# Performance work log

Hardware: AMD Instinct MI355X
Metric: run time of the kernel (lower is better)

Reference implementation:

```python
import jax, jax.numpy as jnp
import numpy as np

B, L, WD = 4096, 30, 300          # batch of news, title length, word dim
H, AD = 20, 20                    # attention heads, per-head dim
MD = H * AD                       # multi_dim = 400
E, ED = 10, 100                   # entities per news, entity dim
QD = 200                          # query_vector_dim
CAT, CD = 18, 50                  # category vocab / dim
SUB, SD = 300, 50                 # subcategory vocab / dim


def _mha(x, wq, bq, wk, bk, wv, bv):
    # x: [B, L, Din] -> [B, L, MD]; standard multi-head self-attention
    b, l, _ = x.shape
    q = (x @ wq + bq).reshape(b, l, H, AD)
    k = (x @ wk + bk).reshape(b, l, H, AD)
    v = (x @ wv + bv).reshape(b, l, H, AD)
    scores = jnp.einsum('blhd,bmhd->bhlm', q, k) / jnp.sqrt(jnp.asarray(AD, x.dtype))
    attn = jax.nn.softmax(scores, axis=-1)
    out = jnp.einsum('bhlm,bmhd->blhd', attn, v)
    return out.reshape(b, l, MD)


def _layernorm(x, g, b):
    mu = jnp.mean(x, axis=-1, keepdims=True)
    var = jnp.var(x, axis=-1, keepdims=True)
    return (x - mu) / jnp.sqrt(var + 1e-5) * g + b


def _additive(x, w, b, q):
    # x: [B, L, D] -> [B, D]
    scores = jnp.tanh(x @ w + b) @ q            # [B, L]
    alpha = jax.nn.softmax(scores, axis=-1)
    return jnp.einsum('bl,bld->bd', alpha, x)


def setup_inputs() -> dict:
    key = jax.random.key(0)
    ks = iter(jax.random.split(key, 40))
    n = lambda shape, s=0.02: (jax.random.normal(next(ks), shape, dtype=jnp.float32) * s)
    inp = {
        'word_embedding': jax.random.normal(next(ks), (B, L, WD), dtype=jnp.float32),
        'entity_embedding': jax.random.normal(next(ks), (B, E, ED), dtype=jnp.float32),
        'category_index': jax.random.randint(next(ks), (B,), 0, CAT, dtype=jnp.int64 if jax.config.jax_enable_x64 else jnp.int32),
        'subcategory_index': jax.random.randint(next(ks), (B,), 0, SUB, dtype=jnp.int64 if jax.config.jax_enable_x64 else jnp.int32),
        # category / subcategory branches
        'emb_cat': n((CAT, CD), 1.0), 'fc1_w': n((CD, MD)), 'fc1_b': jnp.zeros((MD,), jnp.float32),
        'emb_sub': n((SUB, SD), 1.0), 'fc2_w': n((SD, MD)), 'fc2_b': jnp.zeros((MD,), jnp.float32),
        # word multi-head self-attention
        'wq': n((WD, MD)), 'bq': jnp.zeros((MD,), jnp.float32),
        'wk': n((WD, MD)), 'bk': jnp.zeros((MD,), jnp.float32),
        'wv': n((WD, MD)), 'bv': jnp.zeros((MD,), jnp.float32),
        # shared LayerNorm
        'ln_g': jnp.ones((MD,), jnp.float32), 'ln_b': jnp.zeros((MD,), jnp.float32),
        # word additive attention
        'wa_w': n((MD, QD)), 'wa_b': jnp.zeros((QD,), jnp.float32), 'wa_q': n((QD,), 1.0),
        # entity branch: fc3 + GCN (learnable adjacency over the E entities of a news)
        'fc3_w': n((ED, ED)), 'fc3_b': jnp.zeros((ED,), jnp.float32),
        'gcn_A': n((E, E), 1.0), 'gcn_w': n((ED, MD)), 'gcn_b': jnp.zeros((MD,), jnp.float32),
        'ea_w': n((MD, QD)), 'ea_b': jnp.zeros((QD,), jnp.float32), 'ea_q': n((QD,), 1.0),
        # final news-level additive attention over 4 views
        'na_w': n((MD, QD)), 'na_b': jnp.zeros((QD,), jnp.float32), 'na_q': n((QD,), 1.0),
    }
    return inp


def reference(word_embedding, entity_embedding, category_index, subcategory_index,
              emb_cat, fc1_w, fc1_b, emb_sub, fc2_w, fc2_b,
              wq, bq, wk, bk, wv, bv, ln_g, ln_b,
              wa_w, wa_b, wa_q, fc3_w, fc3_b, gcn_A, gcn_w, gcn_b,
              ea_w, ea_b, ea_q, na_w, na_b, na_q):
    # category / subcategory reps (dropout is identity in eval)
    cat_rep = jnp.tanh(emb_cat[category_index] @ fc1_w + fc1_b)      # [B, MD]
    sub_rep = jnp.tanh(emb_sub[subcategory_index] @ fc2_w + fc2_b)   # [B, MD]
    # word branch
    w = _mha(word_embedding, wq, bq, wk, bk, wv, bv)                 # [B, L, MD]
    w = _layernorm(w, ln_g, ln_b)
    word_rep = jnp.tanh(_additive(w, wa_w, wa_b, wa_q))              # [B, MD]
    # entity branch: fc3 -> intra-news GCN -> shared LayerNorm
    e = jnp.tanh(entity_embedding @ fc3_w + fc3_b)                   # [B, E, ED]
    e = jax.nn.relu(jnp.einsum('ef,bfd->bed', gcn_A, e) @ gcn_w + gcn_b)  # [B, E, MD]
    e = _layernorm(e, ln_g, ln_b)
    ent_rep = jnp.tanh(_additive(e, ea_w, ea_b, ea_q))               # [B, MD]
    # fuse the 4 views with additive attention
    views = jnp.stack([word_rep, ent_rep, cat_rep, sub_rep], axis=1)  # [B, 4, MD]
    news_rep = jnp.tanh(_additive(views, na_w, na_b, na_q))          # [B, MD]
    return news_rep
```

## Files before the change

### kernel.cpp

```cpp
#include <hip/hip_runtime.h>
#include <hip/hip_bf16.h>
#include <math.h>

#define B_  4096
#define L_  30
#define WD_ 300
#define H_  20
#define AD_ 20
#define MD_ 400
#define E_  10
#define ED_ 100
#define QD_ 200
#define CD_ 50
#define SD_ 50

typedef unsigned short ushort_t;
typedef __attribute__((ext_vector_type(8))) short bf16x8_t;
typedef __attribute__((ext_vector_type(4))) float f32x4_t;

#define SX_STR   328
#define QKV_STR  1218
#define OUTB_STR 424
#define SOUT_STR 401
#define P_STR    33
#define WT_K     320
#define WAT_K    416

#define N_WT    (1200 * WT_K)
#define N_WAT   (208 * WAT_K)
#define N_FC3T  (112 * 128)
#define N_GCNT  (400 * 128)
#define N_EAT   (208 * WAT_K)

union FragU {
  unsigned  u[4];
  short     s[8];
  bf16x8_t  h;
};

__device__ __forceinline__ ushort_t f2bf(float f) {
  unsigned u = __builtin_bit_cast(unsigned, f);
  unsigned r = (u + 0x7fffu + ((u >> 16) & 1u)) >> 16;
  return (ushort_t)r;
}
__device__ __forceinline__ float bf2f(ushort_t h) {
  return __builtin_bit_cast(float, ((unsigned)h) << 16);
}
__device__ __forceinline__ float wave_reduce_sum(float v) {
  #pragma unroll
  for (int off = 32; off > 0; off >>= 1) v += __shfl_xor(v, off);
  return v;
}
__device__ __forceinline__ void split2(float v, ushort_t* __restrict__ H,
                                       ushort_t* __restrict__ Lo, int idx) {
  const ushort_t h = f2bf(v);
  H[idx] = h;
  Lo[idx] = f2bf(v - bf2f(h));
}

__global__ __launch_bounds__(256) void prep_weights(
    const float* __restrict__ wq, const float* __restrict__ wk, const float* __restrict__ wv,
    const float* __restrict__ wa_w, const float* __restrict__ fc3_w,
    const float* __restrict__ gcn_w, const float* __restrict__ ea_w,
    ushort_t* __restrict__ Wt,
    ushort_t* __restrict__ WatH, ushort_t* __restrict__ WatL,
    ushort_t* __restrict__ fc3TH, ushort_t* __restrict__ fc3TL,
    ushort_t* __restrict__ gcnTH, ushort_t* __restrict__ gcnTL,
    ushort_t* __restrict__ eaTH, ushort_t* __restrict__ eaTL)
{
  int idx = blockIdx.x * 256 + threadIdx.x;
  if (idx < N_WT) {
    const int n = idx / WT_K, k = idx - n * WT_K;
    float v = 0.f;
    if (k < WD_) {
      const float* w = (n < 400) ? wq : (n < 800) ? wk : wv;
      const int c = (n < 400) ? n : (n < 800) ? n - 400 : n - 800;
      v = w[k * MD_ + c];
    }
    Wt[idx] = f2bf(v);
    return;
  }
  idx -= N_WT;
  if (idx < N_WAT) {
    const int q = idx / WAT_K, d = idx - q * WAT_K;
    const float v = (q < QD_ && d < MD_) ? wa_w[d * QD_ + q] : 0.f;
    split2(v, WatH, WatL, idx);
    return;
  }
  idx -= N_WAT;
  if (idx < N_FC3T) {
    const int n = idx / 128, k = idx - n * 128;
    const float v = (n < ED_ && k < ED_) ? fc3_w[k * ED_ + n] : 0.f;
    split2(v, fc3TH, fc3TL, idx);
    return;
  }
  idx -= N_FC3T;
  if (idx < N_GCNT) {
    const int n = idx / 128, k = idx - n * 128;
    const float v = (k < ED_) ? gcn_w[k * MD_ + n] : 0.f;
    split2(v, gcnTH, gcnTL, idx);
    return;
  }
  idx -= N_GCNT;
  if (idx < N_EAT) {
    const int q = idx / WAT_K, d = idx - q * WAT_K;
    const float v = (q < QD_ && d < MD_) ? ea_w[d * QD_ + q] : 0.f;
    split2(v, eaTH, eaTL, idx);
  }
}

__global__ __launch_bounds__(512) void word_branch_kernel(
    const float* __restrict__ X,
    const ushort_t* __restrict__ Wt,
    const ushort_t* __restrict__ WatH, const ushort_t* __restrict__ WatL,
    const float* __restrict__ bq, const float* __restrict__ bk, const float* __restrict__ bv,
    const float* __restrict__ ln_g, const float* __restrict__ ln_b,
    const float* __restrict__ wa_b, const float* __restrict__ wa_q,
    float* __restrict__ word_rep)
{
  __shared__ __align__(16) union {
    ushort_t x[32 * SX_STR];
    float    p[8 * 32 * P_STR];
  } uA;
  __shared__ __align__(16) union {
    ushort_t qkv[32 * QKV_STR];
    struct { ushort_t h[32 * OUTB_STR], l[32 * OUTB_STR]; } o;
  } uB;
  __shared__ __align__(16) float sOut[30 * SOUT_STR];
  __shared__ float sSc[32];
  __shared__ float sAlpha[32];

  const int b    = blockIdx.x;
  const int tid  = threadIdx.x;
  const int wave = tid >> 6;
  const int lane = tid & 63;
  const int lr   = lane & 15;
  const int kg   = lane >> 4;

  const float* xb = X + (size_t)b * (L_ * WD_);
  {
    const int r = tid >> 4, c0 = tid & 15;
    #pragma unroll
    for (int k = 0; k < 20; ++k) {
      const int c = c0 + k * 16;
      const float v = (r < L_ && c < WD_) ? xb[r * WD_ + c] : 0.f;
      uA.x[r * SX_STR + c] = f2bf(v);
    }
  }
  if (tid < 32) sSc[tid] = 0.f;
  __syncthreads();

  for (int jt = wave; jt < 38; jt += 8) {
    const int nt0 = 2 * jt, nt1 = 2 * jt + 1;
    const bool has1 = (nt1 < 75);
    f32x4_t a00 = {0,0,0,0}, a10 = {0,0,0,0}, a01 = {0,0,0,0}, a11 = {0,0,0,0};
    for (int ks = 0; ks < 10; ++ks) {
      const int kb = ks * 32 + kg * 8;
      bf16x8_t af0 = *reinterpret_cast<const bf16x8_t*>(&uA.x[lr * SX_STR + kb]);
      bf16x8_t af1 = *reinterpret_cast<const bf16x8_t*>(&uA.x[(16 + lr) * SX_STR + kb]);
      bf16x8_t bf0 = *reinterpret_cast<const bf16x8_t*>(&Wt[(nt0 * 16 + lr) * WT_K + kb]);
      a00 = __builtin_amdgcn_mfma_f32_16x16x32_bf16(af0, bf0, a00, 0, 0, 0);
      a10 = __builtin_amdgcn_mfma_f32_16x16x32_bf16(af1, bf0, a10, 0, 0, 0);
      if (has1) {
        bf16x8_t bf1 = *reinterpret_cast<const bf16x8_t*>(&Wt[(nt1 * 16 + lr) * WT_K + kb]);
        a01 = __builtin_amdgcn_mfma_f32_16x16x32_bf16(af0, bf1, a01, 0, 0, 0);
        a11 = __builtin_amdgcn_mfma_f32_16x16x32_bf16(af1, bf1, a11, 0, 0, 0);
      }
    }
    #pragma unroll
    for (int half = 0; half < 2; ++half) {
      if (half && !has1) break;
      const int nt = half ? nt1 : nt0;
      const int col = nt * 16 + lr;
      const float bias = (col < 400) ? bq[col] : (col < 800) ? bk[col - 400] : bv[col - 800];
      const f32x4_t am0 = half ? a01 : a00;
      const f32x4_t am1 = half ? a11 : a10;
      #pragma unroll
      for (int i = 0; i < 4; ++i) {
        uB.qkv[(kg * 4 + i) * QKV_STR + col]      = f2bf(am0[i] + bias);
        uB.qkv[(16 + kg * 4 + i) * QKV_STR + col] = f2bf(am1[i] + bias);
      }
    }
  }
  __syncthreads();

  float* pw = &uA.p[wave * (32 * P_STR)];
  for (int h = wave; h < H_; h += 8) {
    const int hq = h * AD_, hk = 400 + h * AD_, hv = 800 + h * AD_;

    bf16x8_t aq[2], bkf[2];
    #pragma unroll
    for (int t = 0; t < 2; ++t) {
      FragU fq, fk;
      fq.u[0]=fq.u[1]=fq.u[2]=fq.u[3]=0;
      fk.u[0]=fk.u[1]=fk.u[2]=fk.u[3]=0;
      if (kg < 3) {
        const ushort_t* pq = &uB.qkv[(t * 16 + lr) * QKV_STR + hq + kg * 8];
        const ushort_t* pk = &uB.qkv[(t * 16 + lr) * QKV_STR + hk + kg * 8];
        fq.u[0] = *(const unsigned*)(pq);     fq.u[1] = *(const unsigned*)(pq + 2);
        fk.u[0] = *(const unsigned*)(pk);     fk.u[1] = *(const unsigned*)(pk + 2);
        if (kg < 2) {
          fq.u[2] = *(const unsigned*)(pq + 4); fq.u[3] = *(const unsigned*)(pq + 6);
          fk.u[2] = *(const unsigned*)(pk + 4); fk.u[3] = *(const unsigned*)(pk + 6);
        }
      }
      aq[t] = fq.h; bkf[t] = fk.h;
    }
    f32x4_t c00 = {0,0,0,0}, c01 = {0,0,0,0}, c10 = {0,0,0,0}, c11 = {0,0,0,0};
    c00 = __builtin_amdgcn_mfma_f32_16x16x32_bf16(aq[0], bkf[0], c00, 0, 0, 0);
    c01 = __builtin_amdgcn_mfma_f32_16x16x32_bf16(aq[0], bkf[1], c01, 0, 0, 0);
    c10 = __builtin_amdgcn_mfma_f32_16x16x32_bf16(aq[1], bkf[0], c10, 0, 0, 0);
    c11 = __builtin_amdgcn_mfma_f32_16x16x32_bf16(aq[1], bkf[1], c11, 0, 0, 0);

    const float SCALE = 0.2236067977499790f;
    #pragma unroll
    for (int mt = 0; mt < 2; ++mt) {
      const f32x4_t v0f = mt ? c10 : c00;
      const f32x4_t v1f = mt ? c11 : c01;
      #pragma unroll
      for (int i = 0; i < 4; ++i) {
        const float v0 = v0f[i] * SCALE;
        const float v1 = (lr < 14) ? v1f[i] * SCALE : -1e30f;
        float mx = fmaxf(v0, v1);
        mx = fmaxf(mx, __shfl_xor(mx, 1));
        mx = fmaxf(mx, __shfl_xor(mx, 2));
        mx = fmaxf(mx, __shfl_xor(mx, 4));
        mx = fmaxf(mx, __shfl_xor(mx, 8));
        const float e0 = __expf(v0 - mx);
        const float e1 = (lr < 14) ? __expf(v1 - mx) : 0.f;
        float s = e0 + e1;
        s += __shfl_xor(s, 1);
        s += __shfl_xor(s, 2);
        s += __shfl_xor(s, 4);
        s += __shfl_xor(s, 8);
        const float inv = 1.f / s;
        const int row = mt * 16 + kg * 4 + i;
        pw[row * P_STR + lr]      = e0 * inv;
        pw[row * P_STR + 16 + lr] = e1 * inv;
      }
    }
    __asm__ volatile("s_waitcnt lgkmcnt(0)" ::: "memory");

    bf16x8_t aph[2], apl[2];
    #pragma unroll
    for (int t = 0; t < 2; ++t) {
      FragU fh, fl;
      #pragma unroll
      for (int j = 0; j < 8; ++j) {
        const float p = pw[(t * 16 + lr) * P_STR + kg * 8 + j];
        const ushort_t hh = f2bf(p);
        fh.s[j] = (short)hh;
        fl.s[j] = (short)f2bf(p - bf2f(hh));
      }
      aph[t] = fh.h; apl[t] = fl.h;
    }
    bf16x8_t bvf[2];
    #pragma unroll
    for (int nt = 0; nt < 2; ++nt) {
      FragU f;
      const int d = nt * 16 + lr;
      if (d < AD_) {
        #pragma unroll
        for (int j = 0; j < 8; ++j)
          f.s[j] = (short)uB.qkv[(kg * 8 + j) * QKV_STR + hv + d];
      } else {
        f.u[0]=f.u[1]=f.u[2]=f.u[3]=0;
      }
      bvf[nt] = f.h;
    }
    f32x4_t o00 = {0,0,0,0}, o01 = {0,0,0,0}, o10 = {0,0,0,0}, o11 = {0,0,0,0};
    o00 = __builtin_amdgcn_mfma_f32_16x16x32_bf16(aph[0], bvf[0], o00, 0, 0, 0);
    o00 = __builtin_amdgcn_mfma_f32_16x16x32_bf16(apl[0], bvf[0], o00, 0, 0, 0);
    o01 = __builtin_amdgcn_mfma_f32_16x16x32_bf16(aph[0], bvf[1], o01, 0, 0, 0);
    o01 = __builtin_amdgcn_mfma_f32_16x16x32_bf16(apl[0], bvf[1], o01, 0, 0, 0);
    o10 = __builtin_amdgcn_mfma_f32_16x16x32_bf16(aph[1], bvf[0], o10, 0, 0, 0);
    o10 = __builtin_amdgcn_mfma_f32_16x16x32_bf16(apl[1], bvf[0], o10, 0, 0, 0);
    o11 = __builtin_amdgcn_mfma_f32_16x16x32_bf16(aph[1], bvf[1], o11, 0, 0, 0);
    o11 = __builtin_amdgcn_mfma_f32_16x16x32_bf16(apl[1], bvf[1], o11, 0, 0, 0);

    #pragma unroll
    for (int mt = 0; mt < 2; ++mt) {
      #pragma unroll
      for (int nt = 0; nt < 2; ++nt) {
        const f32x4_t o = mt ? (nt ? o11 : o10) : (nt ? o01 : o00);
        const int d = nt * 16 + lr;
        if (d < AD_) {
          #pragma unroll
          for (int i = 0; i < 4; ++i) {
            const int r = mt * 16 + kg * 4 + i;
            if (r < L_) sOut[r * SOUT_STR + h * AD_ + d] = o[i];
          }
        }
      }
    }
  }
  __syncthreads();

  for (int r = wave; r < L_; r += 8) {
    float s = 0.f, s2 = 0.f;
    for (int d = lane; d < MD_; d += 64) { const float v = sOut[r * SOUT_STR + d]; s += v; s2 += v * v; }
    s  = wave_reduce_sum(s);
    s2 = wave_reduce_sum(s2);
    const float mu  = s * (1.f / MD_);
    const float var = s2 * (1.f / MD_) - mu * mu;
    const float inv = rsqrtf(var + 1e-5f);
    for (int d = lane; d < MD_; d += 64)
      sOut[r * SOUT_STR + d] = (sOut[r * SOUT_STR + d] - mu) * inv * ln_g[d] + ln_b[d];
  }
  __syncthreads();

  {
    const int r = tid >> 4, c0 = tid & 15;
    #pragma unroll
    for (int k = 0; k < 26; ++k) {
      const int c = c0 + k * 16;
      const float v = (r < L_ && c < MD_) ? sOut[r * SOUT_STR + c] : 0.f;
      const ushort_t hh = f2bf(v);
      uB.o.h[r * OUTB_STR + c] = hh;
      uB.o.l[r * OUTB_STR + c] = f2bf(v - bf2f(hh));
    }
  }
  __syncthreads();

  for (int t = wave; t < 26; t += 8) {
    const int mt = t & 1, nt = t >> 1;
    f32x4_t acc = {0,0,0,0};
    for (int ks = 0; ks < 13; ++ks) {
      const int kb = ks * 32 + kg * 8;
      bf16x8_t ah = *reinterpret_cast<const bf16x8_t*>(&uB.o.h[(mt * 16 + lr) * OUTB_STR + kb]);
      bf16x8_t al = *reinterpret_cast<const bf16x8_t*>(&uB.o.l[(mt * 16 + lr) * OUTB_STR + kb]);
      bf16x8_t wh = *reinterpret_cast<const bf16x8_t*>(&WatH[(nt * 16 + lr) * WAT_K + kb]);
      bf16x8_t wl = *reinterpret_cast<const bf16x8_t*>(&WatL[(nt * 16 + lr) * WAT_K + kb]);
      acc = __builtin_amdgcn_mfma_f32_16x16x32_bf16(ah, wh, acc, 0, 0, 0);
      acc = __builtin_amdgcn_mfma_f32_16x16x32_bf16(al, wh, acc, 0, 0, 0);
      acc = __builtin_amdgcn_mfma_f32_16x16x32_bf16(ah, wl, acc, 0, 0, 0);
    }
    const int q = nt * 16 + lr;
    if (q < QD_) {
      const float bb = wa_b[q], qq = wa_q[q];
      #pragma unroll
      for (int i = 0; i < 4; ++i) {
        const int row = mt * 16 + kg * 4 + i;
        if (row < L_) atomicAdd(&sSc[row], tanhf(acc[i] + bb) * qq);
      }
    }
  }
  __syncthreads();

  if (wave == 0) {
    const float v = (lane < L_) ? sSc[lane] : -1e30f;
    float mx = v;
    #pragma unroll
    for (int off = 32; off > 0; off >>= 1) mx = fmaxf(mx, __shfl_xor(mx, off));
    const float e = (lane < L_) ? __expf(v - mx) : 0.f;
    float s = e;
    #pragma unroll
    for (int off = 32; off > 0; off >>= 1) s += __shfl_xor(s, off);
    if (lane < L_) sAlpha[lane] = e / s;
  }
  __syncthreads();

  for (int d = tid; d < MD_; d += 512) {
    float acc = 0.f;
    #pragma unroll 6
    for (int l = 0; l < L_; ++l) acc += sAlpha[l] * sOut[l * SOUT_STR + d];
    word_rep[(size_t)b * MD_ + d] = tanhf(acc);
  }
}

__global__ __launch_bounds__(256) void entity_branch_kernel(
    const float* __restrict__ Ein,
    const ushort_t* __restrict__ fc3TH, const ushort_t* __restrict__ fc3TL,
    const float* __restrict__ fc3_b,
    const float* __restrict__ gcn_A,
    const ushort_t* __restrict__ gcnTH, const ushort_t* __restrict__ gcnTL,
    const float* __restrict__ gcn_b,
    const float* __restrict__ ln_g, const float* __restrict__ ln_b,
    const ushort_t* __restrict__ eaTH, const ushort_t* __restrict__ eaTL,
    const float* __restrict__ ea_b, const float* __restrict__ ea_q,
    float* __restrict__ ent_rep)
{
  __shared__ __align__(16) ushort_t sEh[16 * 136], sEl[16 * 136];
  __shared__ __align__(16) float    eF[E_ * 104];
  __shared__ __align__(16) ushort_t gH[16 * 136], gL[16 * 136];
  __shared__ __align__(16) float    sR[16 * SOUT_STR];
  __shared__ __align__(16) ushort_t oH[16 * OUTB_STR], oL[16 * OUTB_STR];
  __shared__ float sSc[16];
  __shared__ float sAlpha[16];

  const int b    = blockIdx.x;
  const int tid  = threadIdx.x;
  const int wave = tid >> 6;
  const int lane = tid & 63;
  const int lr   = lane & 15;
  const int kg   = lane >> 4;

  {
    const int r = tid >> 4, c0 = tid & 15;
    #pragma unroll
    for (int k = 0; k < 8; ++k) {
      const int c = c0 + k * 16;
      const float v = (r < E_ && c < ED_) ? Ein[(size_t)b * (E_ * ED_) + r * ED_ + c] : 0.f;
      const ushort_t hh = f2bf(v);
      sEh[r * 136 + c] = hh;
      sEl[r * 136 + c] = f2bf(v - bf2f(hh));
    }
  }
  for (int id = tid; id < 16 * 136; id += 256) { gH[id] = 0; gL[id] = 0; }
  if (tid < 16) sSc[tid] = 0.f;
  __syncthreads();

  for (int nt = wave; nt < 7; nt += 4) {
    f32x4_t acc = {0,0,0,0};
    #pragma unroll
    for (int ks = 0; ks < 4; ++ks) {
      const int kb = ks * 32 + kg * 8;
      bf16x8_t ah = *reinterpret_cast<const bf16x8_t*>(&sEh[lr * 136 + kb]);
      bf16x8_t al = *reinterpret_cast<const bf16x8_t*>(&sEl[lr * 136 + kb]);
      bf16x8_t wh = *reinterpret_cast<const bf16x8_t*>(&fc3TH[(nt * 16 + lr) * 128 + kb]);
      bf16x8_t wl = *reinterpret_cast<const bf16x8_t*>(&fc3TL[(nt * 16 + lr) * 128 + kb]);
      acc = __builtin_amdgcn_mfma_f32_16x16x32_bf16(ah, wh, acc, 0, 0, 0);
      acc = __builtin_amdgcn_mfma_f32_16x16x32_bf16(al, wh, acc, 0, 0, 0);
      acc = __builtin_amdgcn_mfma_f32_16x16x32_bf16(ah, wl, acc, 0, 0, 0);
    }
    const int d = nt * 16 + lr;
    if (d < ED_) {
      const float bias = fc3_b[d];
      #pragma unroll
      for (int i = 0; i < 4; ++i) {
        const int r = kg * 4 + i;
        if (r < E_) eF[r * 104 + d] = tanhf(acc[i] + bias);
      }
    }
  }
  __syncthreads();

  for (int id = tid; id < E_ * ED_; id += 256) {
    const int i = id / ED_, d = id - (id / ED_) * ED_;
    float acc = 0.f;
    #pragma unroll
    for (int f = 0; f < E_; ++f) acc += gcn_A[i * E_ + f] * eF[f * 104 + d];
    const ushort_t hh = f2bf(acc);
    gH[i * 136 + d] = hh;
    gL[i * 136 + d] = f2bf(acc - bf2f(hh));
  }
  __syncthreads();

  for (int nt = wave; nt < 25; nt += 4) {
    f32x4_t acc = {0,0,0,0};
    #pragma unroll
    for (int ks = 0; ks < 4; ++ks) {
      const int kb = ks * 32 + kg * 8;
      bf16x8_t ah = *reinterpret_cast<const bf16x8_t*>(&gH[lr * 136 + kb]);
      bf16x8_t al = *reinterpret_cast<const bf16x8_t*>(&gL[lr * 136 + kb]);
      bf16x8_t wh = *reinterpret_cast<const bf16x8_t*>(&gcnTH[(nt * 16 + lr) * 128 + kb]);
      bf16x8_t wl = *reinterpret_cast<const bf16x8_t*>(&gcnTL[(nt * 16 + lr) * 128 + kb]);
      acc = __builtin_amdgcn_mfma_f32_16x16x32_bf16(ah, wh, acc, 0, 0, 0);
      acc = __builtin_amdgcn_mfma_f32_16x16x32_bf16(al, wh, acc, 0, 0, 0);
      acc = __builtin_amdgcn_mfma_f32_16x16x32_bf16(ah, wl, acc, 0, 0, 0);
    }
    const int d = nt * 16 + lr;
    const float bias = gcn_b[d];
    #pragma unroll
    for (int i = 0; i < 4; ++i) {
      const int r = kg * 4 + i;
      if (r < E_) sR[r * SOUT_STR + d] = fmaxf(acc[i] + bias, 0.f);
    }
  }
  __syncthreads();

  for (int r = wave; r < E_; r += 4) {
    float s = 0.f, s2 = 0.f;
    for (int d = lane; d < MD_; d += 64) { const float v = sR[r * SOUT_STR + d]; s += v; s2 += v * v; }
    s  = wave_reduce_sum(s);
    s2 = wave_reduce_sum(s2);
    const float mu  = s * (1.f / MD_);
    const float var = s2 * (1.f / MD_) - mu * mu;
    const float inv = rsqrtf(var + 1e-5f);
    for (int d = lane; d < MD_; d += 64)
      sR[r * SOUT_STR + d] = (sR[r * SOUT_STR + d] - mu) * inv * ln_g[d] + ln_b[d];
  }
  __syncthreads();

  {
    const int r = tid >> 4, c0 = tid & 15;
    #pragma unroll
    for (int k = 0; k < 26; ++k) {
      const int c = c0 + k * 16;
      const float v = (r < E_ && c < MD_) ? sR[r * SOUT_STR + c] : 0.f;
      const ushort_t hh = f2bf(v);
      oH[r * OUTB_STR + c] = hh;
      oL[r * OUTB_STR + c] = f2bf(v - bf2f(hh));
    }
  }
  __syncthreads();

  for (int nt = wave; nt < 13; nt += 4) {
    f32x4_t acc = {0,0,0,0};
    for (int ks = 0; ks < 13; ++ks) {
      const int kb = ks * 32 + kg * 8;
      bf16x8_t ah = *reinterpret_cast<const bf16x8_t*>(&oH[lr * OUTB_STR + kb]);
      bf16x8_t al = *reinterpret_cast<const bf16x8_t*>(&oL[lr * OUTB_STR + kb]);
      bf16x8_t wh = *reinterpret_cast<const bf16x8_t*>(&eaTH[(nt * 16 + lr) * WAT_K + kb]);
      bf16x8_t wl = *reinterpret_cast<const bf16x8_t*>(&eaTL[(nt * 16 + lr) * WAT_K + kb]);
      acc = __builtin_amdgcn_mfma_f32_16x16x32_bf16(ah, wh, acc, 0, 0, 0);
      acc = __builtin_amdgcn_mfma_f32_16x16x32_bf16(al, wh, acc, 0, 0, 0);
      acc = __builtin_amdgcn_mfma_f32_16x16x32_bf16(ah, wl, acc, 0, 0, 0);
    }
    const int q = nt * 16 + lr;
    if (q < QD_) {
      const float bb = ea_b[q], qq = ea_q[q];
      #pragma unroll
      for (int i = 0; i < 4; ++i) {
        const int r = kg * 4 + i;
        if (r < E_) atomicAdd(&sSc[r], tanhf(acc[i] + bb) * qq);
      }
    }
  }
  __syncthreads();

  if (wave == 0) {
    const float v = (lane < E_) ? sSc[lane] : -1e30f;
    float mx = v;
    #pragma unroll
    for (int off = 32; off > 0; off >>= 1) mx = fmaxf(mx, __shfl_xor(mx, off));
    const float e = (lane < E_) ? __expf(v - mx) : 0.f;
    float s = e;
    #pragma unroll
    for (int off = 32; off > 0; off >>= 1) s += __shfl_xor(s, off);
    if (lane < E_) sAlpha[lane] = e / s;
  }
  __syncthreads();

  for (int d = tid; d < MD_; d += 256) {
    float acc = 0.f;
    #pragma unroll
    for (int i = 0; i < E_; ++i) acc += sAlpha[i] * sR[i * SOUT_STR + d];
    ent_rep[(size_t)b * MD_ + d] = tanhf(acc);
  }
}

__global__ __launch_bounds__(256) void catsub_kernel(
    const int* __restrict__ cat_idx, const int* __restrict__ sub_idx,
    const float* __restrict__ emb_cat, const float* __restrict__ fc1_w, const float* __restrict__ fc1_b,
    const float* __restrict__ emb_sub, const float* __restrict__ fc2_w, const float* __restrict__ fc2_b,
    float* __restrict__ cat_rep, float* __restrict__ sub_rep)
{
  int idx = blockIdx.x * 256 + threadIdx.x;
  const int total = B_ * MD_;
  if (idx < total) {
    const int b = idx / MD_, d = idx - (idx / MD_) * MD_;
    const float* row = emb_cat + (size_t)cat_idx[b] * CD_;
    float acc = fc1_b[d];
    #pragma unroll
    for (int k = 0; k < CD_; ++k) acc += row[k] * fc1_w[k * MD_ + d];
    cat_rep[idx] = tanhf(acc);
  } else {
    idx -= total;
    if (idx < total) {
      const int b = idx / MD_, d = idx - (idx / MD_) * MD_;
      const float* row = emb_sub + (size_t)sub_idx[b] * SD_;
      float acc = fc2_b[d];
      #pragma unroll
      for (int k = 0; k < SD_; ++k) acc += row[k] * fc2_w[k * MD_ + d];
      sub_rep[idx] = tanhf(acc);
    }
  }
}

__global__ __launch_bounds__(256) void fuse_kernel(
    const float* __restrict__ word_rep, const float* __restrict__ ent_rep,
    const float* __restrict__ cat_rep, const float* __restrict__ sub_rep,
    const float* __restrict__ na_w, const float* __restrict__ na_b, const float* __restrict__ na_q,
    float* __restrict__ out)
{
  __shared__ float sViews[4][MD_];
  __shared__ float sSc[4];
  __shared__ float sAlpha[4];
  const int b = blockIdx.x, tid = threadIdx.x;
  for (int d = tid; d < MD_; d += 256) {
    sViews[0][d] = word_rep[(size_t)b * MD_ + d];
    sViews[1][d] = ent_rep[(size_t)b * MD_ + d];
    sViews[2][d] = cat_rep[(size_t)b * MD_ + d];
    sViews[3][d] = sub_rep[(size_t)b * MD_ + d];
  }
  if (tid < 4) sSc[tid] = 0.f;
  __syncthreads();
  for (int id = tid; id < 4 * QD_; id += 256) {
    const int v = id / QD_, q = id - (id / QD_) * QD_;
    float acc = na_b[q];
    #pragma unroll 4
    for (int d = 0; d < MD_; ++d) acc += sViews[v][d] * na_w[d * QD_ + q];
    atomicAdd(&sSc[v], tanhf(acc) * na_q[q]);
  }
  __syncthreads();
  if (tid == 0) {
    float mx = -1e30f;
    for (int v = 0; v < 4; ++v) mx = fmaxf(mx, sSc[v]);
    float sum = 0.f;
    for (int v = 0; v < 4; ++v) { const float e = __expf(sSc[v] - mx); sAlpha[v] = e; sum += e; }
    const float inv = 1.f / sum;
    for (int v = 0; v < 4; ++v) sAlpha[v] *= inv;
  }
  __syncthreads();
  for (int d = tid; d < MD_; d += 256) {
    const float acc = sAlpha[0] * sViews[0][d] + sAlpha[1] * sViews[1][d] +
                      sAlpha[2] * sViews[2][d] + sAlpha[3] * sViews[3][d];
    out[(size_t)b * MD_ + d] = tanhf(acc);
  }
}

extern "C" void kernel_launch(void* const* d_in, const int* in_sizes, int n_in,
                              void* d_out, int out_size, void* d_ws, size_t ws_size,
                              hipStream_t stream) {
  const float* X        = (const float*)d_in[0];
  const float* Ein      = (const float*)d_in[1];
  const int*   cat_idx  = (const int*)d_in[2];
  const int*   sub_idx  = (const int*)d_in[3];
  const float* emb_cat  = (const float*)d_in[4];
  const float* fc1_w    = (const float*)d_in[5];
  const float* fc1_b    = (const float*)d_in[6];
  const float* emb_sub  = (const float*)d_in[7];
  const float* fc2_w    = (const float*)d_in[8];
  const float* fc2_b    = (const float*)d_in[9];
  const float* wq       = (const float*)d_in[10];
  const float* bq       = (const float*)d_in[11];
  const float* wk       = (const float*)d_in[12];
  const float* bk       = (const float*)d_in[13];
  const float* wv       = (const float*)d_in[14];
  const float* bv       = (const float*)d_in[15];
  const float* ln_g     = (const float*)d_in[16];
  const float* ln_b     = (const float*)d_in[17];
  const float* wa_w     = (const float*)d_in[18];
  const float* wa_b     = (const float*)d_in[19];
  const float* wa_q     = (const float*)d_in[20];
  const float* fc3_w    = (const float*)d_in[21];
  const float* fc3_b    = (const float*)d_in[22];
  const float* gcn_A    = (const float*)d_in[23];
  const float* gcn_w    = (const float*)d_in[24];
  const float* gcn_b    = (const float*)d_in[25];
  const float* ea_w     = (const float*)d_in[26];
  const float* ea_b     = (const float*)d_in[27];
  const float* ea_q     = (const float*)d_in[28];
  const float* na_w     = (const float*)d_in[29];
  const float* na_b     = (const float*)d_in[30];
  const float* na_q     = (const float*)d_in[31];

  float* out = (float*)d_out;
  const size_t BM = (size_t)B_ * MD_;
  float* word_rep = (float*)d_ws;
  float* ent_rep  = word_rep + BM;
  float* cat_rep  = ent_rep + BM;
  float* sub_rep  = cat_rep + BM;
  ushort_t* Wt    = (ushort_t*)(sub_rep + BM);
  ushort_t* WatH  = Wt + N_WT;
  ushort_t* WatL  = WatH + N_WAT;
  ushort_t* fc3TH = WatL + N_WAT;
  ushort_t* fc3TL = fc3TH + N_FC3T;
  ushort_t* gcnTH = fc3TL + N_FC3T;
  ushort_t* gcnTL = gcnTH + N_GCNT;
  ushort_t* eaTH  = gcnTL + N_GCNT;
  ushort_t* eaTL  = eaTH + N_EAT;

  {
    const int total = N_WT + N_WAT + N_FC3T + N_GCNT + N_EAT;
    prep_weights<<<(total + 255) / 256, 256, 0, stream>>>(
        wq, wk, wv, wa_w, fc3_w, gcn_w, ea_w,
        Wt, WatH, WatL, fc3TH, fc3TL, gcnTH, gcnTL, eaTH, eaTL);
  }
  word_branch_kernel<<<B_, 512, 0, stream>>>(X, Wt, WatH, WatL, bq, bk, bv,
                                             ln_g, ln_b, wa_b, wa_q, word_rep);
  entity_branch_kernel<<<B_, 256, 0, stream>>>(Ein, fc3TH, fc3TL, fc3_b, gcn_A,
                                               gcnTH, gcnTL, gcn_b,
                                               ln_g, ln_b, eaTH, eaTL, ea_b, ea_q, ent_rep);
  catsub_kernel<<<(2 * B_ * MD_) / 256, 256, 0, stream>>>(cat_idx, sub_idx,
                                                          emb_cat, fc1_w, fc1_b,
                                                          emb_sub, fc2_w, fc2_b,
                                                          cat_rep, sub_rep);
  fuse_kernel<<<B_, 256, 0, stream>>>(word_rep, ent_rep, cat_rep, sub_rep,
                                      na_w, na_b, na_q, out);
}
```

Baseline: 1.500 ms.

## Drop bf16 split precision in word branch and double block sizes

```diff
diff --git a/kernel.cpp b/kernel.cpp
--- a/kernel.cpp
+++ b/kernel.cpp
@@ -22,7 +22,7 @@
 #define QKV_STR  1218
 #define OUTB_STR 424
 #define SOUT_STR 401
-#define P_STR    33
+#define P_STR    40
 #define WT_K     320
 #define WAT_K    416
 
@@ -62,8 +62,7 @@
     const float* __restrict__ wq, const float* __restrict__ wk, const float* __restrict__ wv,
     const float* __restrict__ wa_w, const float* __restrict__ fc3_w,
     const float* __restrict__ gcn_w, const float* __restrict__ ea_w,
-    ushort_t* __restrict__ Wt,
-    ushort_t* __restrict__ WatH, ushort_t* __restrict__ WatL,
+    ushort_t* __restrict__ Wt, ushort_t* __restrict__ Wat,
     ushort_t* __restrict__ fc3TH, ushort_t* __restrict__ fc3TL,
     ushort_t* __restrict__ gcnTH, ushort_t* __restrict__ gcnTL,
     ushort_t* __restrict__ eaTH, ushort_t* __restrict__ eaTL)
@@ -83,8 +82,7 @@
   idx -= N_WT;
   if (idx < N_WAT) {
     const int q = idx / WAT_K, d = idx - q * WAT_K;
-    const float v = (q < QD_ && d < MD_) ? wa_w[d * QD_ + q] : 0.f;
-    split2(v, WatH, WatL, idx);
+    Wat[idx] = (q < QD_ && d < MD_) ? f2bf(wa_w[d * QD_ + q]) : (ushort_t)0;
     return;
   }
   idx -= N_WAT;
@@ -109,10 +107,9 @@
   }
 }
 
-__global__ __launch_bounds__(512) void word_branch_kernel(
+__global__ __launch_bounds__(1024, 4) void word_branch_kernel(
     const float* __restrict__ X,
-    const ushort_t* __restrict__ Wt,
-    const ushort_t* __restrict__ WatH, const ushort_t* __restrict__ WatL,
+    const ushort_t* __restrict__ Wt, const ushort_t* __restrict__ Wat,
     const float* __restrict__ bq, const float* __restrict__ bk, const float* __restrict__ bv,
     const float* __restrict__ ln_g, const float* __restrict__ ln_b,
     const float* __restrict__ wa_b, const float* __restrict__ wa_q,
@@ -120,11 +117,11 @@
 {
   __shared__ __align__(16) union {
     ushort_t x[32 * SX_STR];
-    float    p[8 * 32 * P_STR];
+    ushort_t p[16 * 32 * P_STR];
   } uA;
   __shared__ __align__(16) union {
-    ushort_t qkv[32 * QKV_STR];
-    struct { ushort_t h[32 * OUTB_STR], l[32 * OUTB_STR]; } o;
+    ushort_t qkv[30 * QKV_STR];
+    ushort_t o[32 * OUTB_STR];
   } uB;
   __shared__ __align__(16) float sOut[30 * SOUT_STR];
   __shared__ float sSc[32];
@@ -139,10 +136,11 @@
 
   const float* xb = X + (size_t)b * (L_ * WD_);
   {
-    const int r = tid >> 4, c0 = tid & 15;
-    #pragma unroll
-    for (int k = 0; k < 20; ++k) {
-      const int c = c0 + k * 16;
+    const int r = tid >> 5;
+    const int c0 = tid & 31;
+    #pragma unroll
+    for (int k = 0; k < 10; ++k) {
+      const int c = c0 + k * 32;
       const float v = (r < L_ && c < WD_) ? xb[r * WD_ + c] : 0.f;
       uA.x[r * SX_STR + c] = f2bf(v);
     }
@@ -150,7 +148,7 @@
   if (tid < 32) sSc[tid] = 0.f;
   __syncthreads();
 
-  for (int jt = wave; jt < 38; jt += 8) {
+  for (int jt = wave; jt < 38; jt += 16) {
     const int nt0 = 2 * jt, nt1 = 2 * jt + 1;
     const bool has1 = (nt1 < 75);
     f32x4_t a00 = {0,0,0,0}, a10 = {0,0,0,0}, a01 = {0,0,0,0}, a11 = {0,0,0,0};
@@ -177,15 +175,16 @@
       const f32x4_t am1 = half ? a11 : a10;
       #pragma unroll
       for (int i = 0; i < 4; ++i) {
-        uB.qkv[(kg * 4 + i) * QKV_STR + col]      = f2bf(am0[i] + bias);
-        uB.qkv[(16 + kg * 4 + i) * QKV_STR + col] = f2bf(am1[i] + bias);
-      }
-    }
-  }
-  __syncthreads();
-
-  float* pw = &uA.p[wave * (32 * P_STR)];
-  for (int h = wave; h < H_; h += 8) {
+        uB.qkv[(kg * 4 + i) * QKV_STR + col] = f2bf(am0[i] + bias);
+        const int r2 = 16 + kg * 4 + i;
+        if (r2 < L_) uB.qkv[r2 * QKV_STR + col] = f2bf(am1[i] + bias);
+      }
+    }
+  }
+  __syncthreads();
+
+  ushort_t* pw = &uA.p[wave * (32 * P_STR)];
+  for (int h = wave; h < H_; h += 16) {
     const int hq = h * AD_, hk = 400 + h * AD_, hv = 800 + h * AD_;
 
     bf16x8_t aq[2], bkf[2];
@@ -194,7 +193,8 @@
       FragU fq, fk;
       fq.u[0]=fq.u[1]=fq.u[2]=fq.u[3]=0;
       fk.u[0]=fk.u[1]=fk.u[2]=fk.u[3]=0;
-      if (kg < 3) {
+      const bool okrow = (t == 0) || (lr < 14);
+      if (okrow && kg < 3) {
         const ushort_t* pq = &uB.qkv[(t * 16 + lr) * QKV_STR + hq + kg * 8];
         const ushort_t* pk = &uB.qkv[(t * 16 + lr) * QKV_STR + hk + kg * 8];
         fq.u[0] = *(const unsigned*)(pq);     fq.u[1] = *(const unsigned*)(pq + 2);
@@ -235,25 +235,15 @@
         s += __shfl_xor(s, 8);
         const float inv = 1.f / s;
         const int row = mt * 16 + kg * 4 + i;
-        pw[row * P_STR + lr]      = e0 * inv;
-        pw[row * P_STR + 16 + lr] = e1 * inv;
+        pw[row * P_STR + lr]      = f2bf(e0 * inv);
+        pw[row * P_STR + 16 + lr] = f2bf(e1 * inv);
       }
     }
     __asm__ volatile("s_waitcnt lgkmcnt(0)" ::: "memory");
 
-    bf16x8_t aph[2], apl[2];
-    #pragma unroll
-    for (int t = 0; t < 2; ++t) {
-      FragU fh, fl;
-      #pragma unroll
-      for (int j = 0; j < 8; ++j) {
-        const float p = pw[(t * 16 + lr) * P_STR + kg * 8 + j];
-        const ushort_t hh = f2bf(p);
-        fh.s[j] = (short)hh;
-        fl.s[j] = (short)f2bf(p - bf2f(hh));
-      }
-      aph[t] = fh.h; apl[t] = fl.h;
-    }
+    bf16x8_t ap[2];
+    ap[0] = *reinterpret_cast<const bf16x8_t*>(&pw[lr * P_STR + kg * 8]);
+    ap[1] = *reinterpret_cast<const bf16x8_t*>(&pw[(16 + lr) * P_STR + kg * 8]);
     bf16x8_t bvf[2];
     #pragma unroll
     for (int nt = 0; nt < 2; ++nt) {
@@ -261,22 +251,20 @@
       const int d = nt * 16 + lr;
       if (d < AD_) {
         #pragma unroll
-        for (int j = 0; j < 8; ++j)
-          f.s[j] = (short)uB.qkv[(kg * 8 + j) * QKV_STR + hv + d];
+        for (int j = 0; j < 8; ++j) {
+          const int rm = kg * 8 + j;
+          f.s[j] = (rm < L_) ? (short)uB.qkv[rm * QKV_STR + hv + d] : (short)0;
+        }
       } else {
         f.u[0]=f.u[1]=f.u[2]=f.u[3]=0;
       }
       bvf[nt] = f.h;
     }
     f32x4_t o00 = {0,0,0,0}, o01 = {0,0,0,0}, o10 = {0,0,0,0}, o11 = {0,0,0,0};
-    o00 = __builtin_amdgcn_mfma_f32_16x16x32_bf16(aph[0], bvf[0], o00, 0, 0, 0);
-    o00 = __builtin_amdgcn_mfma_f32_16x16x32_bf16(apl[0], bvf[0], o00, 0, 0, 0);
-    o01 = __builtin_amdgcn_mfma_f32_16x16x32_bf16(aph[0], bvf[1], o01, 0, 0, 0);
-    o01 = __builtin_amdgcn_mfma_f32_16x16x32_bf16(apl[0], bvf[1], o01, 0, 0, 0);
-    o10 = __builtin_amdgcn_mfma_f32_16x16x32_bf16(aph[1], bvf[0], o10, 0, 0, 0);
-    o10 = __builtin_amdgcn_mfma_f32_16x16x32_bf16(apl[1], bvf[0], o10, 0, 0, 0);
-    o11 = __builtin_amdgcn_mfma_f32_16x16x32_bf16(aph[1], bvf[1], o11, 0, 0, 0);
-    o11 = __builtin_amdgcn_mfma_f32_16x16x32_bf16(apl[1], bvf[1], o11, 0, 0, 0);
+    o00 = __builtin_amdgcn_mfma_f32_16x16x32_bf16(ap[0], bvf[0], o00, 0, 0, 0);
+    o01 = __builtin_amdgcn_mfma_f32_16x16x32_bf16(ap[0], bvf[1], o01, 0, 0, 0);
+    o10 = __builtin_amdgcn_mfma_f32_16x16x32_bf16(ap[1], bvf[0], o10, 0, 0, 0);
+    o11 = __builtin_amdgcn_mfma_f32_16x16x32_bf16(ap[1], bvf[1], o11, 0, 0, 0);
 
     #pragma unroll
     for (int mt = 0; mt < 2; ++mt) {
@@ -296,7 +284,7 @@
   }
   __syncthreads();
 
-  for (int r = wave; r < L_; r += 8) {
+  for (int r = wave; r < L_; r += 16) {
     float s = 0.f, s2 = 0.f;
     for (int d = lane; d < MD_; d += 64) { const float v = sOut[r * SOUT_STR + d]; s += v; s2 += v * v; }
     s  = wave_reduce_sum(s);
@@ -310,30 +298,27 @@
   __syncthreads();
 
   {
-    const int r = tid >> 4, c0 = tid & 15;
-    #pragma unroll
-    for (int k = 0; k < 26; ++k) {
-      const int c = c0 + k * 16;
-      const float v = (r < L_ && c < MD_) ? sOut[r * SOUT_STR + c] : 0.f;
-      const ushort_t hh = f2bf(v);
-      uB.o.h[r * OUTB_STR + c] = hh;
-      uB.o.l[r * OUTB_STR + c] = f2bf(v - bf2f(hh));
-    }
-  }
-  __syncthreads();
-
-  for (int t = wave; t < 26; t += 8) {
+    const int r = tid >> 5;
+    const int c0 = tid & 31;
+    #pragma unroll
+    for (int k = 0; k < 13; ++k) {
+      const int c = c0 + k * 32;
+      if (c < 416) {
+        const float v = (r < L_ && c < MD_) ? sOut[r * SOUT_STR + c] : 0.f;
+        uB.o[r * OUTB_STR + c] = f2bf(v);
+      }
+    }
+  }
+  __syncthreads();
+
+  for (int t = wave; t < 26; t += 16) {
     const int mt = t & 1, nt = t >> 1;
     f32x4_t acc = {0,0,0,0};
     for (int ks = 0; ks < 13; ++ks) {
       const int kb = ks * 32 + kg * 8;
-      bf16x8_t ah = *reinterpret_cast<const bf16x8_t*>(&uB.o.h[(mt * 16 + lr) * OUTB_STR + kb]);
-      bf16x8_t al = *reinterpret_cast<const bf16x8_t*>(&uB.o.l[(mt * 16 + lr) * OUTB_STR + kb]);
-      bf16x8_t wh = *reinterpret_cast<const bf16x8_t*>(&WatH[(nt * 16 + lr) * WAT_K + kb]);
-      bf16x8_t wl = *reinterpret_cast<const bf16x8_t*>(&WatL[(nt * 16 + lr) * WAT_K + kb]);
-      acc = __builtin_amdgcn_mfma_f32_16x16x32_bf16(ah, wh, acc, 0, 0, 0);
-      acc = __builtin_amdgcn_mfma_f32_16x16x32_bf16(al, wh, acc, 0, 0, 0);
-      acc = __builtin_amdgcn_mfma_f32_16x16x32_bf16(ah, wl, acc, 0, 0, 0);
+      bf16x8_t af = *reinterpret_cast<const bf16x8_t*>(&uB.o[(mt * 16 + lr) * OUTB_STR + kb]);
+      bf16x8_t wf = *reinterpret_cast<const bf16x8_t*>(&Wat[(nt * 16 + lr) * WAT_K + kb]);
+      acc = __builtin_amdgcn_mfma_f32_16x16x32_bf16(af, wf, acc, 0, 0, 0);
     }
     const int q = nt * 16 + lr;
     if (q < QD_) {
@@ -360,7 +345,8 @@
   }
   __syncthreads();
 
-  for (int d = tid; d < MD_; d += 512) {
+  if (tid < MD_) {
+    const int d = tid;
     float acc = 0.f;
     #pragma unroll 6
     for (int l = 0; l < L_; ++l) acc += sAlpha[l] * sOut[l * SOUT_STR + d];
@@ -368,7 +354,7 @@
   }
 }
 
-__global__ __launch_bounds__(256) void entity_branch_kernel(
+__global__ __launch_bounds__(512, 4) void entity_branch_kernel(
     const float* __restrict__ Ein,
     const ushort_t* __restrict__ fc3TH, const ushort_t* __restrict__ fc3TL,
     const float* __restrict__ fc3_b,
@@ -395,22 +381,18 @@
   const int lr   = lane & 15;
   const int kg   = lane >> 4;
 
-  {
-    const int r = tid >> 4, c0 = tid & 15;
-    #pragma unroll
-    for (int k = 0; k < 8; ++k) {
-      const int c = c0 + k * 16;
-      const float v = (r < E_ && c < ED_) ? Ein[(size_t)b * (E_ * ED_) + r * ED_ + c] : 0.f;
-      const ushort_t hh = f2bf(v);
-      sEh[r * 136 + c] = hh;
-      sEl[r * 136 + c] = f2bf(v - bf2f(hh));
-    }
-  }
-  for (int id = tid; id < 16 * 136; id += 256) { gH[id] = 0; gL[id] = 0; }
+  for (int id = tid; id < 16 * 128; id += 512) {
+    const int r = id >> 7, c = id & 127;
+    const float v = (r < E_ && c < ED_) ? Ein[(size_t)b * (E_ * ED_) + r * ED_ + c] : 0.f;
+    const ushort_t hh = f2bf(v);
+    sEh[r * 136 + c] = hh;
+    sEl[r * 136 + c] = f2bf(v - bf2f(hh));
+  }
+  for (int id = tid; id < 16 * 136; id += 512) { gH[id] = 0; gL[id] = 0; }
   if (tid < 16) sSc[tid] = 0.f;
   __syncthreads();
 
-  for (int nt = wave; nt < 7; nt += 4) {
+  for (int nt = wave; nt < 7; nt += 8) {
     f32x4_t acc = {0,0,0,0};
     #pragma unroll
     for (int ks = 0; ks < 4; ++ks) {
@@ -435,7 +417,7 @@
   }
   __syncthreads();
 
-  for (int id = tid; id < E_ * ED_; id += 256) {
+  for (int id = tid; id < E_ * ED_; id += 512) {
     const int i = id / ED_, d = id - (id / ED_) * ED_;
     float acc = 0.f;
     #pragma unroll
@@ -446,7 +428,7 @@
   }
   __syncthreads();
 
-  for (int nt = wave; nt < 25; nt += 4) {
+  for (int nt = wave; nt < 25; nt += 8) {
     f32x4_t acc = {0,0,0,0};
     #pragma unroll
     for (int ks = 0; ks < 4; ++ks) {
@@ -469,7 +451,7 @@
   }
   __syncthreads();
 
-  for (int r = wave; r < E_; r += 4) {
+  for (int r = wave; r < E_; r += 8) {
     float s = 0.f, s2 = 0.f;
     for (int d = lane; d < MD_; d += 64) { const float v = sR[r * SOUT_STR + d]; s += v; s2 += v * v; }
     s  = wave_reduce_sum(s);
@@ -483,10 +465,11 @@
   __syncthreads();
 
   {
-    const int r = tid >> 4, c0 = tid & 15;
-    #pragma unroll
-    for (int k = 0; k < 26; ++k) {
-      const int c = c0 + k * 16;
+    const int r = tid >> 5;
+    const int c0 = tid & 31;
+    #pragma unroll
+    for (int k = 0; k < 13; ++k) {
+      const int c = c0 + k * 32;
       const float v = (r < E_ && c < MD_) ? sR[r * SOUT_STR + c] : 0.f;
       const ushort_t hh = f2bf(v);
       oH[r * OUTB_STR + c] = hh;
@@ -495,7 +478,7 @@
   }
   __syncthreads();
 
-  for (int nt = wave; nt < 13; nt += 4) {
+  for (int nt = wave; nt < 13; nt += 8) {
     f32x4_t acc = {0,0,0,0};
     for (int ks = 0; ks < 13; ++ks) {
       const int kb = ks * 32 + kg * 8;
@@ -532,7 +515,8 @@
   }
   __syncthreads();
 
-  for (int d = tid; d < MD_; d += 256) {
+  if (tid < MD_) {
+    const int d = tid;
     float acc = 0.f;
     #pragma unroll
     for (int i = 0; i < E_; ++i) acc += sAlpha[i] * sR[i * SOUT_STR + d];
@@ -653,9 +637,8 @@
   float* cat_rep  = ent_rep + BM;
   float* sub_rep  = cat_rep + BM;
   ushort_t* Wt    = (ushort_t*)(sub_rep + BM);
-  ushort_t* WatH  = Wt + N_WT;
-  ushort_t* WatL  = WatH + N_WAT;
-  ushort_t* fc3TH = WatL + N_WAT;
+  ushort_t* Wat   = Wt + N_WT;
+  ushort_t* fc3TH = Wat + N_WAT;
   ushort_t* fc3TL = fc3TH + N_FC3T;
   ushort_t* gcnTH = fc3TL + N_FC3T;
   ushort_t* gcnTL = gcnTH + N_GCNT;
@@ -666,11 +649,11 @@
     const int total = N_WT + N_WAT + N_FC3T + N_GCNT + N_EAT;
     prep_weights<<<(total + 255) / 256, 256, 0, stream>>>(
         wq, wk, wv, wa_w, fc3_w, gcn_w, ea_w,
-        Wt, WatH, WatL, fc3TH, fc3TL, gcnTH, gcnTL, eaTH, eaTL);
-  }
-  word_branch_kernel<<<B_, 512, 0, stream>>>(X, Wt, WatH, WatL, bq, bk, bv,
-                                             ln_g, ln_b, wa_b, wa_q, word_rep);
-  entity_branch_kernel<<<B_, 256, 0, stream>>>(Ein, fc3TH, fc3TL, fc3_b, gcn_A,
+        Wt, Wat, fc3TH, fc3TL, gcnTH, gcnTL, eaTH, eaTL);
+  }
+  word_branch_kernel<<<B_, 1024, 0, stream>>>(X, Wt, Wat, bq, bk, bv,
+                                              ln_g, ln_b, wa_b, wa_q, word_rep);
+  entity_branch_kernel<<<B_, 512, 0, stream>>>(Ein, fc3TH, fc3TL, fc3_b, gcn_A,
                                                gcnTH, gcnTL, gcn_b,
                                                ln_g, ln_b, eaTH, eaTL, ea_b, ea_q, ent_rep);
   catsub_kernel<<<(2 * B_ * MD_) / 256, 256, 0, stream>>>(cat_idx, sub_idx,
```

Result: faster. 1.326 ms (-11.6%).
